# Optimization experiments

Measured on AMD Instinct MI355X. Metric: run time of the kernel, lower is better.

Reference implementation:

```python
import jax, jax.numpy as jnp
import numpy as np

LAMBDA = 0.1


def setup_inputs() -> dict:
    key = jax.random.key(0)
    k1, k2 = jax.random.split(key)
    shape = (32, 1, 1024, 1024)  # [B, C, H, W], H/W power of 2 (required by the quadtree recursion)
    D_est = jax.random.uniform(k1, shape, dtype=jnp.float32)
    D_gt = jax.random.uniform(k2, shape, dtype=jnp.float32)
    return {"D_est": D_est, "D_gt": D_gt}


def reference(D_est, D_gt):
    # recursive_search bottoms out at 1x1 regions; crowd_count sums over ALL
    # dims (batch/channel included), so for power-of-2 spatial dims the mask
    # is exactly a per-pixel comparison of batch+channel-summed counts,
    # broadcast back over batch/channel.
    s_est = jnp.sum(D_est, axis=(0, 1))  # [H, W]
    s_gt = jnp.sum(D_gt, axis=(0, 1))    # [H, W]
    mask = (s_est > s_gt).astype(D_est.dtype)  # broadcasts over [B, C, H, W]

    diff2 = jnp.sum(jnp.square(D_est - D_gt))          # ||D_est - D_gt||^2
    G2 = jnp.sum(jnp.square(D_est))                    # ||G||^2
    H2 = jnp.sum(jnp.square(D_est * mask))             # ||H||^2
    return diff2 / G2 + LAMBDA * (diff2 / H2)
```

## Files before the change

### kernel.cpp

```cpp
#include <hip/hip_runtime.h>

constexpr int B  = 32;
constexpr int HW = 1024 * 1024;

__global__ __launch_bounds__(256) void pra_main_kernel(
    const float* __restrict__ est,
    const float* __restrict__ gt,
    double* __restrict__ acc)
{
    const int pix4 = blockIdx.x * blockDim.x + threadIdx.x;
    const float4* est4 = reinterpret_cast<const float4*>(est);
    const float4* gt4  = reinterpret_cast<const float4*>(gt);

    float4 se = make_float4(0.f, 0.f, 0.f, 0.f);
    float4 sg = make_float4(0.f, 0.f, 0.f, 0.f);
    float4 q  = make_float4(0.f, 0.f, 0.f, 0.f);
    float  d2 = 0.f;

    #pragma unroll 4
    for (int b = 0; b < B; ++b) {
        const size_t idx = (size_t)b * (HW / 4) + pix4;
        float4 e = est4[idx];
        float4 g = gt4[idx];
        se.x += e.x; se.y += e.y; se.z += e.z; se.w += e.w;
        sg.x += g.x; sg.y += g.y; sg.z += g.z; sg.w += g.w;
        q.x  += e.x * e.x; q.y += e.y * e.y; q.z += e.z * e.z; q.w += e.w * e.w;
        float dx = e.x - g.x, dy = e.y - g.y, dz = e.z - g.z, dw = e.w - g.w;
        d2 += dx * dx + dy * dy + dz * dz + dw * dw;
    }

    float g2 = q.x + q.y + q.z + q.w;
    float h2 = (se.x > sg.x ? q.x : 0.f) + (se.y > sg.y ? q.y : 0.f) +
               (se.z > sg.z ? q.z : 0.f) + (se.w > sg.w ? q.w : 0.f);

    #pragma unroll
    for (int off = 32; off > 0; off >>= 1) {
        d2 += __shfl_down(d2, off);
        g2 += __shfl_down(g2, off);
        h2 += __shfl_down(h2, off);
    }

    __shared__ float sd[4], sG[4], sH[4];
    const int wave = threadIdx.x >> 6;
    const int lane = threadIdx.x & 63;
    if (lane == 0) { sd[wave] = d2; sG[wave] = g2; sH[wave] = h2; }
    __syncthreads();
    if (threadIdx.x == 0) {
        float D = sd[0] + sd[1] + sd[2] + sd[3];
        float G = sG[0] + sG[1] + sG[2] + sG[3];
        float H = sH[0] + sH[1] + sH[2] + sH[3];
        atomicAdd(&acc[0], (double)D);
        atomicAdd(&acc[1], (double)G);
        atomicAdd(&acc[2], (double)H);
    }
}

__global__ void pra_final_kernel(const double* __restrict__ acc,
                                 float* __restrict__ out)
{
    if (threadIdx.x == 0 && blockIdx.x == 0) {
        double d2 = acc[0], g2 = acc[1], h2 = acc[2];
        out[0] = (float)(d2 / g2 + 0.1 * (d2 / h2));
    }
}

extern "C" void kernel_launch(void* const* d_in, const int* in_sizes, int n_in,
                              void* d_out, int out_size, void* d_ws, size_t ws_size,
                              hipStream_t stream)
{
    const float* d_est = (const float*)d_in[0];
    const float* d_gt  = (const float*)d_in[1];
    float* out = (float*)d_out;
    double* acc = (double*)d_ws;

    hipMemsetAsync(acc, 0, 3 * sizeof(double), stream);

    const int threads = 256;
    const int grid = (HW / 4) / threads;
    pra_main_kernel<<<grid, threads, 0, stream>>>(d_est, d_gt, acc);
    pra_final_kernel<<<1, 64, 0, stream>>>(acc, out);
}
```

Baseline: 297.1 us.

## Split batch reduction across threads in a block and combine via LDS

Each block now handles 128 pixel-quads with 4 thread groups, each summing a quarter of the batch, and partial sums are combined through shared memory before the mask test. Loads are batched four at a time to raise memory-level parallelism. The mask now tests the summed difference against zero, which removes one accumulator. This adds an extra LDS exchange and sync, and the compare may round slightly differently from the original.

```diff
diff --git a/kernel.cpp b/kernel.cpp
--- a/kernel.cpp
+++ b/kernel.cpp
@@ -1,37 +1,67 @@
 #include <hip/hip_runtime.h>
 
-constexpr int B  = 32;
-constexpr int HW = 1024 * 1024;
+constexpr int B   = 32;
+constexpr int HW  = 1024 * 1024;
+constexpr int NP4 = HW / 4;
+constexpr int SPLIT = 4;
+constexpr int PT  = 128;
+constexpr int TPB = SPLIT * PT;
+constexpr int BPT = B / SPLIT;
 
-__global__ __launch_bounds__(256) void pra_main_kernel(
+__global__ __launch_bounds__(TPB) void pra_main_kernel(
     const float* __restrict__ est,
     const float* __restrict__ gt,
     double* __restrict__ acc)
 {
-    const int pix4 = blockIdx.x * blockDim.x + threadIdx.x;
+    const int t = threadIdx.x & (PT - 1);
+    const int s = threadIdx.x / PT;
+    const int pix4 = blockIdx.x * PT + t;
     const float4* est4 = reinterpret_cast<const float4*>(est);
     const float4* gt4  = reinterpret_cast<const float4*>(gt);
 
-    float4 se = make_float4(0.f, 0.f, 0.f, 0.f);
-    float4 sg = make_float4(0.f, 0.f, 0.f, 0.f);
-    float4 q  = make_float4(0.f, 0.f, 0.f, 0.f);
-    float  d2 = 0.f;
+    float4 dse = make_float4(0.f, 0.f, 0.f, 0.f);
+    float4 q   = make_float4(0.f, 0.f, 0.f, 0.f);
+    float  d2  = 0.f;
 
-    #pragma unroll 4
-    for (int b = 0; b < B; ++b) {
-        const size_t idx = (size_t)b * (HW / 4) + pix4;
-        float4 e = est4[idx];
-        float4 g = gt4[idx];
-        se.x += e.x; se.y += e.y; se.z += e.z; se.w += e.w;
-        sg.x += g.x; sg.y += g.y; sg.z += g.z; sg.w += g.w;
-        q.x  += e.x * e.x; q.y += e.y * e.y; q.z += e.z * e.z; q.w += e.w * e.w;
-        float dx = e.x - g.x, dy = e.y - g.y, dz = e.z - g.z, dw = e.w - g.w;
-        d2 += dx * dx + dy * dy + dz * dz + dw * dw;
+    const int b0 = s * BPT;
+    #pragma unroll
+    for (int half = 0; half < BPT / 4; ++half) {
+        float4 e[4], g[4];
+        #pragma unroll
+        for (int j = 0; j < 4; ++j) {
+            const size_t idx = (size_t)(b0 + half * 4 + j) * NP4 + pix4;
+            e[j] = est4[idx];
+            g[j] = gt4[idx];
+        }
+        #pragma unroll
+        for (int j = 0; j < 4; ++j) {
+            float dx = e[j].x - g[j].x, dy = e[j].y - g[j].y;
+            float dz = e[j].z - g[j].z, dw = e[j].w - g[j].w;
+            dse.x += dx; dse.y += dy; dse.z += dz; dse.w += dw;
+            q.x += e[j].x * e[j].x; q.y += e[j].y * e[j].y;
+            q.z += e[j].z * e[j].z; q.w += e[j].w * e[j].w;
+            d2 += dx * dx + dy * dy + dz * dz + dw * dw;
+        }
     }
 
+    __shared__ float4 Ldse[SPLIT - 1][PT];
+    __shared__ float4 Lq[SPLIT - 1][PT];
+    if (s > 0) { Ldse[s - 1][t] = dse; Lq[s - 1][t] = q; }
+    __syncthreads();
+
     float g2 = q.x + q.y + q.z + q.w;
-    float h2 = (se.x > sg.x ? q.x : 0.f) + (se.y > sg.y ? q.y : 0.f) +
-               (se.z > sg.z ? q.z : 0.f) + (se.w > sg.w ? q.w : 0.f);
+    float h2 = 0.f;
+    if (s == 0) {
+        float4 dt = dse, qt = q;
+        #pragma unroll
+        for (int k = 0; k < SPLIT - 1; ++k) {
+            float4 a = Ldse[k][t], b4 = Lq[k][t];
+            dt.x += a.x; dt.y += a.y; dt.z += a.z; dt.w += a.w;
+            qt.x += b4.x; qt.y += b4.y; qt.z += b4.z; qt.w += b4.w;
+        }
+        h2 = (dt.x > 0.f ? qt.x : 0.f) + (dt.y > 0.f ? qt.y : 0.f) +
+             (dt.z > 0.f ? qt.z : 0.f) + (dt.w > 0.f ? qt.w : 0.f);
+    }
 
     #pragma unroll
     for (int off = 32; off > 0; off >>= 1) {
@@ -39,16 +69,15 @@
         g2 += __shfl_down(g2, off);
         h2 += __shfl_down(h2, off);
     }
-
-    __shared__ float sd[4], sG[4], sH[4];
+    __shared__ float rd[TPB / 64], rg[TPB / 64], rh[TPB / 64];
     const int wave = threadIdx.x >> 6;
     const int lane = threadIdx.x & 63;
-    if (lane == 0) { sd[wave] = d2; sG[wave] = g2; sH[wave] = h2; }
+    if (lane == 0) { rd[wave] = d2; rg[wave] = g2; rh[wave] = h2; }
     __syncthreads();
     if (threadIdx.x == 0) {
-        float D = sd[0] + sd[1] + sd[2] + sd[3];
-        float G = sG[0] + sG[1] + sG[2] + sG[3];
-        float H = sH[0] + sH[1] + sH[2] + sH[3];
+        float D = 0.f, G = 0.f, H = 0.f;
+        #pragma unroll
+        for (int k = 0; k < TPB / 64; ++k) { D += rd[k]; G += rg[k]; H += rh[k]; }
         atomicAdd(&acc[0], (double)D);
         atomicAdd(&acc[1], (double)G);
         atomicAdd(&acc[2], (double)H);
@@ -75,8 +104,7 @@
 
     hipMemsetAsync(acc, 0, 3 * sizeof(double), stream);
 
-    const int threads = 256;
-    const int grid = (HW / 4) / threads;
-    pra_main_kernel<<<grid, threads, 0, stream>>>(d_est, d_gt, acc);
+    const int grid = NP4 / PT;
+    pra_main_kernel<<<grid, TPB, 0, stream>>>(d_est, d_gt, acc);
     pra_final_kernel<<<1, 64, 0, stream>>>(acc, out);
 }
```

Measured after the change: 287.5 us. -3.2%, faster.
